# Kernel optimization log

Hardware: AMD Instinct MI355X
Metric: run time of the kernel (lower is better)

## Reference

```python
import jax, jax.numpy as jnp
import numpy as np

B, S, D, H = 2, 2048, 1024, 16
HD = D // H  # head_dim = 64


def setup_inputs() -> dict:
    key = jax.random.key(0)
    ks = jax.random.split(key, 9)
    xav = float(np.sqrt(6.0 / (D + D)))  # xavier_uniform bound for square matrices
    def lin_w(k):
        return jax.random.uniform(k, (D, D), jnp.float32, -xav, xav)
    return {
        "x": jax.random.normal(ks[0], (B, S, D), jnp.float32),
        "mask": jnp.ones((B, S), jnp.int32),
        "Wq": lin_w(ks[1]), "bq": jnp.zeros((D,), jnp.float32),
        "Wk": lin_w(ks[2]), "bk": jnp.zeros((D,), jnp.float32),
        "Wv": lin_w(ks[3]), "bv": jnp.zeros((D,), jnp.float32),
        "Wo": lin_w(ks[4]), "bo": jnp.zeros((D,), jnp.float32),
    }


def reference(x, mask, Wq, bq, Wk, bk, Wv, bv, Wo, bo):
    # Linear projections (torch Linear: y = x @ W.T + b)
    q = x @ Wq.T + bq
    k = x @ Wk.T + bk
    v = x @ Wv.T + bv
    # [B, S, D] -> [B, H, S, HD]
    q = q.reshape(B, S, H, HD).transpose(0, 2, 1, 3)
    k = k.reshape(B, S, H, HD).transpose(0, 2, 1, 3)
    v = v.reshape(B, S, H, HD).transpose(0, 2, 1, 3)
    scores = jnp.einsum("bhqd,bhkd->bhqk", q, k) / jnp.sqrt(jnp.float32(HD))
    # mask [B, S] -> [B, 1, 1, S]; masked_fill where mask == 0
    m = mask[:, None, None, :]
    scores = jnp.where(m == 0, jnp.float32(-1e9), scores)
    attn = jax.nn.softmax(scores, axis=-1)
    # dropout in eval mode = identity
    out = jnp.einsum("bhqk,bhkd->bhqd", attn, v)
    out = out.transpose(0, 2, 1, 3).reshape(B, S, D)
    return out @ Wo.T + bo
```

## Files before the change

kernel.cpp:

```cpp
#include <hip/hip_runtime.h>
#include <stdint.h>

#define B_   2
#define S_   2048
#define D_   1024
#define H_   16
#define HD_  64
#define NTOK (B_ * S_)

typedef unsigned short u16;
typedef __bf16 bf16x8 __attribute__((ext_vector_type(8)));
typedef float  f32x4  __attribute__((ext_vector_type(4)));
typedef u16    u16x4  __attribute__((ext_vector_type(4)));
typedef unsigned int u32x2 __attribute__((ext_vector_type(2)));

#define QSCALE 0.180336880f
#define MAXC 4.0f

#if __has_builtin(__builtin_amdgcn_exp2f)
#define EXP2(x) __builtin_amdgcn_exp2f(x)
#else
#define EXP2(x) exp2f(x)
#endif

#define OFF_FLAG ((size_t)0)
#define OFF_BIAS ((size_t)64)
#define OFF_MB   ((size_t)32768)
#define OFF_MF   ((size_t)49152)
#define OFF_X    ((size_t)65536)
#define SZ_X     ((size_t)NTOK * D_ * 2)
#define OFF_W    (OFF_X + SZ_X)
#define SZ_W     ((size_t)D_ * D_ * 2)
#define OFF_Q    (OFF_W + 4 * SZ_W)
#define SZ_T     SZ_X
#define OFF_K2   (OFF_Q + SZ_T)
#define OFF_VT   (OFF_K2 + SZ_T)
#define OFF_AO   (OFF_VT + SZ_T)

__device__ __forceinline__ float bf2f(u16 h) {
    union { uint32_t u; float f; } c; c.u = ((uint32_t)h) << 16; return c.f;
}
__device__ __forceinline__ u16 f2bf(float f) {
    union { float f; uint32_t u; } c; c.f = f;
    uint32_t r = c.u + 0x7fffu + ((c.u >> 16) & 1u);
    return (u16)(r >> 16);
}
__device__ __forceinline__ void glds16(const u16* g, u16* l) {
    __builtin_amdgcn_global_load_lds(
        (const __attribute__((address_space(1))) uint32_t*)g,
        (__attribute__((address_space(3))) uint32_t*)l,
        16, 0, 0);
}
__device__ __forceinline__ f32x4 mfma16(bf16x8 a, bf16x8 b, f32x4 c) {
    return __builtin_amdgcn_mfma_f32_16x16x32_bf16(a, b, c, 0, 0, 0);
}
__device__ __forceinline__ uint32_t pk_bf_trunc(float f0, float f1) {
    return __builtin_amdgcn_perm(__builtin_bit_cast(uint32_t, f1),
                                 __builtin_bit_cast(uint32_t, f0), 0x07060302u);
}
__device__ __forceinline__ void plswap32(uint32_t& a, uint32_t& b) {
#if __has_builtin(__builtin_amdgcn_permlane32_swap)
    u32x2 r = __builtin_amdgcn_permlane32_swap(a, b, false, false);
    a = r[0]; b = r[1];
#else
    asm volatile("s_nop 1\n\tv_permlane32_swap_b32 %0, %1\n\ts_nop 1"
                 : "+v"(a), "+v"(b));
#endif
}
__device__ __forceinline__ void plswap16(uint32_t& a, uint32_t& b) {
#if __has_builtin(__builtin_amdgcn_permlane16_swap)
    u32x2 r = __builtin_amdgcn_permlane16_swap(a, b, false, false);
    a = r[0]; b = r[1];
#else
    asm volatile("s_nop 1\n\tv_permlane16_swap_b32 %0, %1\n\ts_nop 1"
                 : "+v"(a), "+v"(b));
#endif
}

__global__ void convert_kernel(const void* x, const void* wq, const void* wk,
                               const void* wv, const void* wo,
                               const void* bq, const void* bk, const void* bv,
                               const void* bo, const int* mask, char* ws) {
    __shared__ int s_ok;
    const int tid = threadIdx.x;
    if (tid == 0) s_ok = 1;
    __syncthreads();
    {
        const u16* p = (const u16*)wq;
        bool bad = false;
        for (int j = 0; j < 8; ++j) {
            float v = bf2f(p[(tid * 8 + j) * 2]);
            if (!(v > -1.0f && v < 1.0f)) bad = true;
        }
        if (bad) s_ok = 0;
    }
    __syncthreads();
    const int is_bf16 = s_ok;
    if (blockIdx.x == 0 && tid == 0) *(int*)(ws + OFF_FLAG) = is_bf16;

    const uint32_t NX = (uint32_t)NTOK * D_;
    const uint32_t NW = (uint32_t)D_ * D_;
    if (!is_bf16) {
        u16* Xd = (u16*)(ws + OFF_X);
        u16* Wd = (u16*)(ws + OFF_W);
        for (uint32_t i = blockIdx.x * 256u + tid; i < NX + 4 * NW;
             i += gridDim.x * 256u) {
            const void* src; uint32_t si; u16* dst;
            if (i < NX) { src = x; si = i; dst = Xd + i; }
            else {
                uint32_t j = i - NX;
                uint32_t w = j >> 20; si = j & (NW - 1u);
                src = (w == 0) ? wq : (w == 1) ? wk : (w == 2) ? wv : wo;
                dst = Wd + j;
            }
            *dst = f2bf(((const float*)src)[si]);
        }
    }
    float* Bd = (float*)(ws + OFF_BIAS);
    float* Mbd = (float*)(ws + OFF_MB);
    int* MFd = (int*)(ws + OFF_MF);
    const uint32_t NB = 4u * D_;
    const uint32_t total2 = NB + (uint32_t)NTOK + B_ * 32;
    for (uint32_t i = blockIdx.x * 256u + tid; i < total2;
         i += gridDim.x * 256u) {
        if (i < NB) {
            uint32_t w = i >> 10; uint32_t si = i & (D_ - 1u);
            const void* src = (w == 0) ? bq : (w == 1) ? bk : (w == 2) ? bv : bo;
            Bd[i] = is_bf16 ? bf2f(((const u16*)src)[si]) : ((const float*)src)[si];
        } else if (i < NB + (uint32_t)NTOK) {
            uint32_t j = i - NB;
            Mbd[j] = (mask[j] == 0) ? -1.0e9f : 0.0f;
        } else {
            uint32_t f = i - NB - (uint32_t)NTOK;
            uint32_t bb = f >> 5, kt = f & 31;
            int any = 0;
            for (int e = 0; e < 64; ++e)
                any |= (mask[bb * S_ + kt * 64 + e] == 0);
            MFd[f] = any;
        }
    }
}

__global__ void qkv_gemm(char* ws, const void* x, const void* wq,
                         const void* wk, const void* wv) {
    __shared__ alignas(16) u16 As[128 * 32];
    __shared__ alignas(16) u16 Bs[128 * 32];
    const int z = blockIdx.z;
    const int is_bf16 = *(const int*)(ws + OFF_FLAG);
    const u16* X = is_bf16 ? (const u16*)x : (const u16*)(ws + OFF_X);
    const u16* W;
    if (is_bf16) W = (z == 0) ? (const u16*)wq : (z == 1) ? (const u16*)wk : (const u16*)wv;
    else         W = (const u16*)(ws + OFF_W + (size_t)z * SZ_W);
    const float* bias = (const float*)(ws + OFF_BIAS) + z * D_;
    u16* Qd  = (u16*)(ws + OFF_Q);
    u16* Kd  = (u16*)(ws + OFF_K2);
    u16* Vtd = (u16*)(ws + OFF_VT);

    const int tid = threadIdx.x, lane = tid & 63, wave = tid >> 6;
    const int wm = (wave & 1) * 64, wn = (wave >> 1) * 64;
    const int lr = lane & 15, quad = lane >> 4;
    const int srow = tid >> 2;
    const int scol = (((tid & 3) ^ ((tid >> 3) & 3)) * 8);
    const int rd_off = (quad ^ ((lr >> 1) & 3)) * 8;

    const u16* Araw; const u16* Braw; int m0, n0;
    if (z < 2) { Araw = W; Braw = X; m0 = blockIdx.x * 128; n0 = blockIdx.y * 128; }
    else       { Araw = X; Braw = W; m0 = blockIdx.y * 128; n0 = blockIdx.x * 128; }

    f32x4 acc[4][4];
#pragma unroll
    for (int i = 0; i < 4; i++)
#pragma unroll
        for (int j = 0; j < 4; j++) acc[i][j] = (f32x4){0.f, 0.f, 0.f, 0.f};

    const u16* Ag0 = Araw + (size_t)(m0 + srow)      * D_ + scol;
    const u16* Ag1 = Araw + (size_t)(m0 + srow + 64) * D_ + scol;
    const u16* Bg0 = Braw + (size_t)(n0 + srow)      * D_ + scol;
    const u16* Bg1 = Braw + (size_t)(n0 + srow + 64) * D_ + scol;

    for (int k0 = 0; k0 < D_; k0 += 32) {
        glds16(Ag0 + k0, &As[tid * 8]);
        glds16(Ag1 + k0, &As[2048 + tid * 8]);
        glds16(Bg0 + k0, &Bs[tid * 8]);
        glds16(Bg1 + k0, &Bs[2048 + tid * 8]);
        __syncthreads();
        bf16x8 a[4], b[4];
#pragma unroll
        for (int i = 0; i < 4; i++) a[i] = *(const bf16x8*)&As[(wm + i * 16 + lr) * 32 + rd_off];
#pragma unroll
        for (int j = 0; j < 4; j++) b[j] = *(const bf16x8*)&Bs[(wn + j * 16 + lr) * 32 + rd_off];
#pragma unroll
        for (int i = 0; i < 4; i++)
#pragma unroll
            for (int j = 0; j < 4; j++) acc[i][j] = mfma16(a[i], b[j], acc[i][j]);
        __syncthreads();
    }

    if (z < 2) {
        u16* dst0 = (z == 0) ? Qd : Kd;
        const float sc_ = (z == 0) ? QSCALE : 1.0f;
#pragma unroll
        for (int i = 0; i < 4; i++) {
            const int fb = m0 + wm + i * 16 + quad * 4;
            const f32x4 b4 = *(const f32x4*)&bias[fb];
            const int h = fb >> 6, hd0 = fb & 63;
#pragma unroll
            for (int j = 0; j < 4; j++) {
                const int tok = n0 + wn + j * 16 + lr;
                const int bb = tok >> 11, s = tok & 2047;
                u16x4 pk;
#pragma unroll
                for (int r = 0; r < 4; r++) pk[r] = f2bf((acc[i][j][r] + b4[r]) * sc_);
                *(u16x4*)&dst0[(((size_t)(bb * H_ + h)) * S_ + s) * HD_ + hd0] = pk;
            }
        }
    } else {
#pragma unroll
        for (int i = 0; i < 4; i++) {
            const int row_b = m0 + wm + i * 16 + quad * 4;
            const int bb = row_b >> 11, s0 = row_b & 2047;
#pragma unroll
            for (int j = 0; j < 4; j++) {
                const int col = n0 + wn + j * 16 + lr;
                const float bv_ = bias[col];
                const int h = col >> 6, hd = col & 63;
                u16x4 pk;
#pragma unroll
                for (int r = 0; r < 4; r++) pk[r] = f2bf(acc[i][j][r] + bv_);
                *(u16x4*)&Vtd[(((size_t)(bb * H_ + h)) * HD_ + hd) * S_ + s0] = pk;
            }
        }
    }
}

__global__ void __launch_bounds__(256, 4)
attn_kernel(char* ws) {
    __shared__ alignas(16) char smem[32768];

    const u16* Qb  = (const u16*)(ws + OFF_Q);
    const u16* Kb  = (const u16*)(ws + OFF_K2);
    const u16* Vtb = (const u16*)(ws + OFF_VT);
    const float* Mb = (const float*)(ws + OFF_MB);
    const int* MF = (const int*)(ws + OFF_MF);
    u16* AO = (u16*)(ws + OFF_AO);

    const int tid = threadIdx.x, lane = tid & 63, wave = tid >> 6;
    const int kc = wave >> 1, qhalf = wave & 1;
    const int bh = blockIdx.y, b = bh >> 4, h = bh & 15;
    const int qb = blockIdx.x * 64 + qhalf * 32;
    const int lr = lane & 15, quad = lane >> 4;
    const int sx = lr & 7;

    const u16* Qbh = Qb  + (size_t)bh * S_ * HD_;
    const u16* Kbh = Kb  + (size_t)bh * S_ * HD_;
    const u16* Vbh = Vtb + (size_t)bh * HD_ * S_;
    const float* Mbb = Mb + b * S_;
    const int* MFb = MF + b * 32;

    u16* Ks  = (u16*)(smem + kc * 8192);
    u16* Vts = (u16*)(smem + 16384 + kc * 8192);

    const int tidh = tid & 127;
    const int st_r = tidh >> 3;
    const int st_c = (tidh & 7) ^ (st_r & 7);
    const u16* Kst = Kbh + (size_t)(kc * 1024 + st_r) * HD_ + st_c * 8;
    const u16* Vst = Vbh + (size_t)st_r * S_ + kc * 1024 + st_c * 8;

    bf16x8 qf[2][2];
#pragma unroll
    for (int s = 0; s < 2; ++s)
#pragma unroll
        for (int hf = 0; hf < 2; ++hf)
            qf[s][hf] = *(const bf16x8*)&Qbh[(size_t)(qb + s * 16 + lr) * HD_ + hf * 32 + quad * 8];

    bf16x8 ones8;
#pragma unroll
    for (int i = 0; i < 8; ++i) ones8[i] = (__bf16)1.0f;

    const f32x4 initm = (f32x4){-MAXC, -MAXC, -MAXC, -MAXC};

    f32x4 oacc[2][4], lacc[2];
#pragma unroll
    for (int s = 0; s < 2; ++s) {
        lacc[s] = (f32x4){0.f, 0.f, 0.f, 0.f};
#pragma unroll
        for (int j = 0; j < 4; ++j) oacc[s][j] = (f32x4){0.f, 0.f, 0.f, 0.f};
    }

    for (int it = 0; it < 16; ++it) {
        const int k0 = kc * 1024 + it * 64;
#pragma unroll
        for (int t = 0; t < 4; ++t) {
            glds16(Kst + (size_t)(it * 64 + t * 16) * HD_, &Ks[(tidh + t * 128) * 8]);
            glds16(Vst + (size_t)t * 16 * S_ + it * 64,    &Vts[(tidh + t * 128) * 8]);
        }
        __syncthreads();

        f32x4 sc[2][4];
#pragma unroll
        for (int j = 0; j < 4; ++j) {
            const int krow = (j * 16 + lr) * 64;
            bf16x8 kfA = *(const bf16x8*)&Ks[krow + ((quad    ) ^ sx) * 8];
            bf16x8 kfB = *(const bf16x8*)&Ks[krow + ((quad + 4) ^ sx) * 8];
#pragma unroll
            for (int s = 0; s < 2; ++s) {
                f32x4 t0 = mfma16(kfA, qf[s][0], initm);
                sc[s][j] = mfma16(kfB, qf[s][1], t0);
            }
        }
        if (MFb[kc * 16 + it]) {
#pragma unroll
            for (int j = 0; j < 4; ++j) {
                const f32x4 mb = *(const f32x4*)&Mbb[k0 + j * 16 + quad * 4];
#pragma unroll
                for (int s = 0; s < 2; ++s) sc[s][j] += mb;
            }
        }
        bf16x8 vf[4][2];
#pragma unroll
        for (int j2 = 0; j2 < 4; ++j2) {
            const int vrow = (j2 * 16 + lr) * 64;
            vf[j2][0] = *(const bf16x8*)&Vts[vrow + ((quad    ) ^ sx) * 8];
            vf[j2][1] = *(const bf16x8*)&Vts[vrow + ((quad + 4) ^ sx) * 8];
        }

#pragma unroll
        for (int s = 0; s < 2; ++s) {
            uint32_t ulo[4], uhi[4];
#pragma unroll
            for (int j = 0; j < 4; ++j) {
                f32x4 p;
#pragma unroll
                for (int r = 0; r < 4; ++r) p[r] = EXP2(sc[s][j][r]);
                ulo[j] = pk_bf_trunc(p[0], p[1]);
                uhi[j] = pk_bf_trunc(p[2], p[3]);
            }
            bf16x8 pf[2];
#pragma unroll
            for (int half = 0; half < 2; ++half) {
                uint32_t x0 = ulo[2 * half], y0 = ulo[2 * half + 1];
                uint32_t x1 = uhi[2 * half], y1 = uhi[2 * half + 1];
                plswap32(x0, y0); plswap16(x0, y0);
                plswap32(x1, y1); plswap16(x1, y1);
                union { uint32_t u[4]; bf16x8 v; } cvt;
                cvt.u[0] = x0;
                cvt.u[1] = x1;
                cvt.u[2] = y0;
                cvt.u[3] = y1;
                pf[half] = cvt.v;
            }
            lacc[s] = mfma16(ones8, pf[0], lacc[s]);
            lacc[s] = mfma16(ones8, pf[1], lacc[s]);
#pragma unroll
            for (int j2 = 0; j2 < 4; ++j2) {
                oacc[s][j2] = mfma16(vf[j2][0], pf[0], oacc[s][j2]);
                oacc[s][j2] = mfma16(vf[j2][1], pf[1], oacc[s][j2]);
            }
        }
        __syncthreads();
    }

    float* Oex = (float*)smem;
    float* lex = (float*)(smem + 17408);
    if (kc == 1) {
#pragma unroll
        for (int s = 0; s < 2; ++s) {
            const int row = qhalf * 32 + s * 16 + lr;
#pragma unroll
            for (int j2 = 0; j2 < 4; ++j2)
                *(f32x4*)&Oex[row * 68 + j2 * 16 + quad * 4] = oacc[s][j2];
            if (quad == 0) lex[row] = lacc[s][0];
        }
    }
    __syncthreads();
    if (kc == 0) {
#pragma unroll
        for (int s = 0; s < 2; ++s) {
            const int row = qhalf * 32 + s * 16 + lr;
            const float linv = 1.0f / (lacc[s][0] + lex[row]);
            const int q = qb + s * 16 + lr;
            u16* dst = AO + (size_t)(b * S_ + q) * D_ + h * HD_ + quad * 4;
#pragma unroll
            for (int j2 = 0; j2 < 4; ++j2) {
                const f32x4 o2 = *(const f32x4*)&Oex[row * 68 + j2 * 16 + quad * 4];
                u16x4 pk;
#pragma unroll
                for (int r = 0; r < 4; ++r) pk[r] = f2bf((oacc[s][j2][r] + o2[r]) * linv);
                *(u16x4*)&dst[j2 * 16] = pk;
            }
        }
    }
}

__global__ void out_gemm(char* ws, const void* wo, void* dout) {
    __shared__ alignas(16) u16 As[128 * 32];
    __shared__ alignas(16) u16 Bs[64 * 32];
    const int is_bf16 = *(const int*)(ws + OFF_FLAG);
    const u16* A  = (const u16*)(ws + OFF_AO);
    const u16* Bt = is_bf16 ? (const u16*)wo : (const u16*)(ws + OFF_W + 3 * SZ_W);
    const float* bias = (const float*)(ws + OFF_BIAS) + 3 * D_;

    const int tid = threadIdx.x, lane = tid & 63, wave = tid >> 6;
    const int wm = (wave & 1) * 64, wn = (wave >> 1) * 32;
    const int m0 = blockIdx.y * 128, n0 = blockIdx.x * 64;
    const int lr = lane & 15, quad = lane >> 4;
    const int srow = tid >> 2;
    const int scol = (((tid & 3) ^ ((tid >> 3) & 3)) * 8);
    const int rd_off = (quad ^ ((lr >> 1) & 3)) * 8;

    f32x4 acc[4][2];
#pragma unroll
    for (int i = 0; i < 4; i++)
#pragma unroll
        for (int j = 0; j < 2; j++) acc[i][j] = (f32x4){0.f, 0.f, 0.f, 0.f};

    const u16* Ag0 = A  + (size_t)(m0 + srow)      * D_ + scol;
    const u16* Ag1 = A  + (size_t)(m0 + srow + 64) * D_ + scol;
    const u16* Bg0 = Bt + (size_t)(n0 + srow)      * D_ + scol;

    for (int k0 = 0; k0 < D_; k0 += 32) {
        glds16(Ag0 + k0, &As[tid * 8]);
        glds16(Ag1 + k0, &As[2048 + tid * 8]);
        glds16(Bg0 + k0, &Bs[tid * 8]);
        __syncthreads();
        bf16x8 a[4], b[2];
#pragma unroll
        for (int i = 0; i < 4; i++) a[i] = *(const bf16x8*)&As[(wm + i * 16 + lr) * 32 + rd_off];
#pragma unroll
        for (int j = 0; j < 2; j++) b[j] = *(const bf16x8*)&Bs[(wn + j * 16 + lr) * 32 + rd_off];
#pragma unroll
        for (int i = 0; i < 4; i++)
#pragma unroll
            for (int j = 0; j < 2; j++) acc[i][j] = mfma16(a[i], b[j], acc[i][j]);
        __syncthreads();
    }
#pragma unroll
    for (int i = 0; i < 4; i++) {
        const int row_b = m0 + wm + i * 16 + quad * 4;
#pragma unroll
        for (int j = 0; j < 2; j++) {
            const int col = n0 + wn + j * 16 + lr;
            const float bv_ = bias[col];
#pragma unroll
            for (int r = 0; r < 4; r++) {
                const int row = row_b + r;
                const float v = acc[i][j][r] + bv_;
                const size_t idx = (size_t)row * D_ + col;
                if (is_bf16) ((u16*)dout)[idx] = f2bf(v);
                else         ((float*)dout)[idx] = v;
            }
        }
    }
}

extern "C" void kernel_launch(void* const* d_in, const int* in_sizes, int n_in,
                              void* d_out, int out_size, void* d_ws, size_t ws_size,
                              hipStream_t stream) {
    (void)in_sizes; (void)n_in; (void)out_size; (void)ws_size;
    const void* x  = d_in[0];
    const int* mask = (const int*)d_in[1];
    const void* wq = d_in[2]; const void* bq = d_in[3];
    const void* wk = d_in[4]; const void* bk = d_in[5];
    const void* wv = d_in[6]; const void* bv = d_in[7];
    const void* wo = d_in[8]; const void* bo = d_in[9];
    char* ws = (char*)d_ws;

    convert_kernel<<<dim3(2048), dim3(256), 0, stream>>>(x, wq, wk, wv, wo,
                                                         bq, bk, bv, bo, mask, ws);
    qkv_gemm<<<dim3(8, 32, 3), dim3(256), 0, stream>>>(ws, x, wq, wk, wv);
    attn_kernel<<<dim3(S_ / 64, B_ * H_), dim3(256), 0, stream>>>(ws);
    out_gemm<<<dim3(16, 32), dim3(256), 0, stream>>>(ws, wo, d_out);
}
```

Before: 216.6 us.

## Double-buffer K/V tiles, drop split-K merge, and remap attention blocks

The attention kernel no longer splits the key range across wave pairs and merges the halves through shared memory. Each of the four waves now owns 32 query rows and walks all 2048 keys, with K/V tiles double-buffered in LDS so the next tile loads while the current one is computed. The grid becomes a 1D launch of 512 blocks, each covering 128 queries, with a swizzled block-to-(head, query tile) mapping. s_setprio is raised around the MFMA sections and launch bounds drop to 2 blocks per CU, which allows more registers but halves the block count and may reduce occupancy.

```diff
diff --git a/kernel.cpp b/kernel.cpp
--- a/kernel.cpp
+++ b/kernel.cpp
@@ -233,7 +233,7 @@
     }
 }
 
-__global__ void __launch_bounds__(256, 4)
+__global__ void __launch_bounds__(256, 2)
 attn_kernel(char* ws) {
     __shared__ alignas(16) char smem[32768];
 
@@ -245,9 +245,10 @@
     u16* AO = (u16*)(ws + OFF_AO);
 
     const int tid = threadIdx.x, lane = tid & 63, wave = tid >> 6;
-    const int kc = wave >> 1, qhalf = wave & 1;
-    const int bh = blockIdx.y, b = bh >> 4, h = bh & 15;
-    const int qb = blockIdx.x * 64 + qhalf * 32;
+    const int lin = blockIdx.x;
+    const int work = (lin & 7) * 64 + (lin >> 3);
+    const int bh = work >> 4, b = bh >> 4, h = bh & 15;
+    const int qb = (work & 15) * 128 + wave * 32;
     const int lr = lane & 15, quad = lane >> 4;
     const int sx = lr & 7;
 
@@ -257,14 +258,15 @@
     const float* Mbb = Mb + b * S_;
     const int* MFb = MF + b * 32;
 
-    u16* Ks  = (u16*)(smem + kc * 8192);
-    u16* Vts = (u16*)(smem + 16384 + kc * 8192);
-
-    const int tidh = tid & 127;
-    const int st_r = tidh >> 3;
-    const int st_c = (tidh & 7) ^ (st_r & 7);
-    const u16* Kst = Kbh + (size_t)(kc * 1024 + st_r) * HD_ + st_c * 8;
-    const u16* Vst = Vbh + (size_t)st_r * S_ + kc * 1024 + st_c * 8;
+    u16* Ks0  = (u16*)(smem);
+    u16* Vts0 = (u16*)(smem + 8192);
+    u16* Ks1  = (u16*)(smem + 16384);
+    u16* Vts1 = (u16*)(smem + 24576);
+
+    const int st_r = tid >> 3;
+    const int st_c = (tid & 7) ^ (st_r & 7);
+    const u16* Kst = Kbh + (size_t)st_r * HD_ + st_c * 8;
+    const u16* Vst = Vbh + (size_t)st_r * S_ + st_c * 8;
 
     bf16x8 qf[2][2];
 #pragma unroll
@@ -287,16 +289,20 @@
         for (int j = 0; j < 4; ++j) oacc[s][j] = (f32x4){0.f, 0.f, 0.f, 0.f};
     }
 
-    for (int it = 0; it < 16; ++it) {
-        const int k0 = kc * 1024 + it * 64;
-#pragma unroll
-        for (int t = 0; t < 4; ++t) {
-            glds16(Kst + (size_t)(it * 64 + t * 16) * HD_, &Ks[(tidh + t * 128) * 8]);
-            glds16(Vst + (size_t)t * 16 * S_ + it * 64,    &Vts[(tidh + t * 128) * 8]);
-        }
-        __syncthreads();
-
+    auto STAGE = [&](int it2, u16* Kd, u16* Vd) {
+        const u16* kg = Kst + (size_t)it2 * 64 * HD_;
+        const u16* vg = Vst + it2 * 64;
+#pragma unroll
+        for (int t = 0; t < 2; ++t) {
+            glds16(kg + (size_t)t * 32 * HD_, &Kd[(t * 256 + tid) * 8]);
+            glds16(vg + (size_t)t * 32 * S_,  &Vd[(t * 256 + tid) * 8]);
+        }
+    };
+
+    auto COMPUTE = [&](int it, const u16* Ks, const u16* Vts) {
+        const int k0 = it * 64;
         f32x4 sc[2][4];
+        __builtin_amdgcn_s_setprio(1);
 #pragma unroll
         for (int j = 0; j < 4; ++j) {
             const int krow = (j * 16 + lr) * 64;
@@ -308,7 +314,8 @@
                 sc[s][j] = mfma16(kfB, qf[s][1], t0);
             }
         }
-        if (MFb[kc * 16 + it]) {
+        __builtin_amdgcn_s_setprio(0);
+        if (MFb[it]) {
 #pragma unroll
             for (int j = 0; j < 4; ++j) {
                 const f32x4 mb = *(const f32x4*)&Mbb[k0 + j * 16 + quad * 4];
@@ -349,6 +356,7 @@
                 cvt.u[3] = y1;
                 pf[half] = cvt.v;
             }
+            __builtin_amdgcn_s_setprio(1);
             lacc[s] = mfma16(ones8, pf[0], lacc[s]);
             lacc[s] = mfma16(ones8, pf[1], lacc[s]);
 #pragma unroll
@@ -356,38 +364,32 @@
                 oacc[s][j2] = mfma16(vf[j2][0], pf[0], oacc[s][j2]);
                 oacc[s][j2] = mfma16(vf[j2][1], pf[1], oacc[s][j2]);
             }
-        }
-        __syncthreads();
-    }
-
-    float* Oex = (float*)smem;
-    float* lex = (float*)(smem + 17408);
-    if (kc == 1) {
-#pragma unroll
-        for (int s = 0; s < 2; ++s) {
-            const int row = qhalf * 32 + s * 16 + lr;
-#pragma unroll
-            for (int j2 = 0; j2 < 4; ++j2)
-                *(f32x4*)&Oex[row * 68 + j2 * 16 + quad * 4] = oacc[s][j2];
-            if (quad == 0) lex[row] = lacc[s][0];
-        }
-    }
-    __syncthreads();
-    if (kc == 0) {
-#pragma unroll
-        for (int s = 0; s < 2; ++s) {
-            const int row = qhalf * 32 + s * 16 + lr;
-            const float linv = 1.0f / (lacc[s][0] + lex[row]);
-            const int q = qb + s * 16 + lr;
-            u16* dst = AO + (size_t)(b * S_ + q) * D_ + h * HD_ + quad * 4;
-#pragma unroll
-            for (int j2 = 0; j2 < 4; ++j2) {
-                const f32x4 o2 = *(const f32x4*)&Oex[row * 68 + j2 * 16 + quad * 4];
-                u16x4 pk;
-#pragma unroll
-                for (int r = 0; r < 4; ++r) pk[r] = f2bf((oacc[s][j2][r] + o2[r]) * linv);
-                *(u16x4*)&dst[j2 * 16] = pk;
-            }
+            __builtin_amdgcn_s_setprio(0);
+        }
+    };
+
+    STAGE(0, Ks0, Vts0);
+    for (int itp = 0; itp < 16; ++itp) {
+        const int itA = 2 * itp, itB = 2 * itp + 1;
+        __syncthreads();
+        STAGE(itB, Ks1, Vts1);
+        COMPUTE(itA, Ks0, Vts0);
+        __syncthreads();
+        if (itA + 2 < 32) STAGE(itA + 2, Ks0, Vts0);
+        COMPUTE(itB, Ks1, Vts1);
+    }
+
+#pragma unroll
+    for (int s = 0; s < 2; ++s) {
+        const float linv = 1.0f / lacc[s][0];
+        const int q = qb + s * 16 + lr;
+        u16* dst = AO + (size_t)(b * S_ + q) * D_ + h * HD_ + quad * 4;
+#pragma unroll
+        for (int j2 = 0; j2 < 4; ++j2) {
+            u16x4 pk;
+#pragma unroll
+            for (int r = 0; r < 4; ++r) pk[r] = f2bf(oacc[s][j2][r] * linv);
+            *(u16x4*)&dst[j2 * 16] = pk;
         }
     }
 }
@@ -468,6 +470,6 @@
     convert_kernel<<<dim3(2048), dim3(256), 0, stream>>>(x, wq, wk, wv, wo,
                                                          bq, bk, bv, bo, mask, ws);
     qkv_gemm<<<dim3(8, 32, 3), dim3(256), 0, stream>>>(ws, x, wq, wk, wv);
-    attn_kernel<<<dim3(S_ / 64, B_ * H_), dim3(256), 0, stream>>>(ws);
+    attn_kernel<<<dim3(512), dim3(256), 0, stream>>>(ws);
     out_gemm<<<dim3(16, 32), dim3(256), 0, stream>>>(ws, wo, d_out);
 }
```

Result: faster. 206.5 us (-4.7%).
